# Performance work log

Measured on AMD Instinct MI355X. Metric: run time of the kernel, lower is better.

Reference implementation:

```python
import jax, jax.numpy as jnp
import numpy as np

B, T_CACHE, N_STATE, N_HEAD = 128, 448, 1280, 20
HEAD_DIM = N_STATE // N_HEAD


def setup_inputs() -> dict:
    key = jax.random.key(0)
    ks = jax.random.split(key, 10)
    s = 1.0 / np.sqrt(N_STATE)
    return {
        "x": jax.random.normal(ks[0], (B, 1, N_STATE), jnp.float32),
        "k_cache": jax.random.normal(ks[1], (B, T_CACHE, N_STATE), jnp.float32),
        "v_cache": jax.random.normal(ks[2], (B, T_CACHE, N_STATE), jnp.float32),
        "mask": jnp.zeros((1, T_CACHE), jnp.float32),
        "Wq": jax.random.normal(ks[3], (N_STATE, N_STATE), jnp.float32) * s,
        "bq": jax.random.normal(ks[4], (N_STATE,), jnp.float32) * s,
        "Wk": jax.random.normal(ks[5], (N_STATE, N_STATE), jnp.float32) * s,
        "Wv": jax.random.normal(ks[6], (N_STATE, N_STATE), jnp.float32) * s,
        "bv": jax.random.normal(ks[7], (N_STATE,), jnp.float32) * s,
        "Wo": jax.random.normal(ks[8], (N_STATE, N_STATE), jnp.float32) * s,
        "bo": jax.random.normal(ks[9], (N_STATE,), jnp.float32) * s,
    }


def reference(x, k_cache, v_cache, mask, Wq, bq, Wk, Wv, bv, Wo, bo):
    b, q_len, n_state = x.shape  # q_len == 1 in loop (streaming) mode
    h, d = N_HEAD, n_state // N_HEAD

    # Q/K/V projections (Whisper: key has no bias)
    q = x @ Wq + bq                         # [B, 1, n_state]
    k = x @ Wk                              # [B, 1, n_state]
    v = x @ Wv + bv                         # [B, 1, n_state]

    # streaming KV-cache shift-and-append
    k_cache = jnp.concatenate([k_cache[:, 1:, :], k], axis=1)  # [B, T, n_state]
    v_cache = jnp.concatenate([v_cache[:, 1:, :], v], axis=1)

    t = k_cache.shape[1]
    scale = d ** (-0.25)
    qh = q.reshape(b, q_len, h, d).transpose(0, 2, 1, 3) * scale   # [B, H, q, d]
    kh = k_cache.reshape(b, t, h, d).transpose(0, 2, 3, 1) * scale  # [B, H, d, T]
    vh = v_cache.reshape(b, t, h, d).transpose(0, 2, 1, 3)          # [B, H, T, d]

    qk = jnp.matmul(qh, kh) + mask          # [B, H, q, T]
    qk = qk.astype(jnp.float32)
    w = jax.nn.softmax(qk, axis=-1).astype(qh.dtype)
    wv = jnp.matmul(w, vh)                  # [B, H, q, d]
    wv = wv.transpose(0, 2, 1, 3).reshape(b, q_len, n_state)

    out = wv @ Wo + bo                      # [B, q, n_state]
    return out, k_cache, v_cache
```

## Files before the change

kernel.cpp:

```cpp
#include <hip/hip_runtime.h>
#include <cstddef>

#define NSTATE 1280
#define TCACHE 448
#define NBATCH 128
#define NHEAD  20
#define HDIM   64
#define NT     8
#define RPC    (TCACHE / NT)

typedef float f4 __attribute__((ext_vector_type(4)));

__device__ __forceinline__ void gemm_body(const float* __restrict__ A,
                                          const float* __restrict__ B,
                                          const float* __restrict__ bias,
                                          float* __restrict__ C, size_t ldc,
                                          int kb, int ke, float scale)
{
    __shared__ float As[32][64];
    __shared__ float Bs[32][32];
    const int tid = threadIdx.x;
    const int m0 = blockIdx.y * 64;
    const int n0 = blockIdx.x * 32;
    const int tr = tid >> 4;
    const int tc = tid & 15;
    float acc[4][2] = {{0.f,0.f},{0.f,0.f},{0.f,0.f},{0.f,0.f}};

    for (int k0 = kb; k0 < ke; k0 += 32) {
        #pragma unroll
        for (int j = 0; j < 2; ++j) {
            int chunk = tid * 2 + j;
            int row   = chunk >> 3;
            int kc    = (chunk & 7) << 2;
            float4 a = *(const float4*)(A + (size_t)(m0 + row) * NSTATE + k0 + kc);
            As[kc+0][row] = a.x; As[kc+1][row] = a.y;
            As[kc+2][row] = a.z; As[kc+3][row] = a.w;
        }
        {
            int row = tid >> 3;
            int nc  = (tid & 7) << 2;
            float4 b4 = *(const float4*)(B + (size_t)(k0 + row) * NSTATE + n0 + nc);
            *(float4*)&Bs[row][nc] = b4;
        }
        __syncthreads();
        #pragma unroll
        for (int kk = 0; kk < 32; ++kk) {
            float4 a = *(const float4*)&As[kk][tr << 2];
            float2 b = *(const float2*)&Bs[kk][tc << 1];
            acc[0][0] = fmaf(a.x, b.x, acc[0][0]); acc[0][1] = fmaf(a.x, b.y, acc[0][1]);
            acc[1][0] = fmaf(a.y, b.x, acc[1][0]); acc[1][1] = fmaf(a.y, b.y, acc[1][1]);
            acc[2][0] = fmaf(a.z, b.x, acc[2][0]); acc[2][1] = fmaf(a.z, b.y, acc[2][1]);
            acc[3][0] = fmaf(a.w, b.x, acc[3][0]); acc[3][1] = fmaf(a.w, b.y, acc[3][1]);
        }
        __syncthreads();
    }
    const int n = n0 + (tc << 1);
    const float b0 = bias ? bias[n]   : 0.f;
    const float b1 = bias ? bias[n+1] : 0.f;
    #pragma unroll
    for (int i = 0; i < 4; ++i) {
        size_t m = (size_t)(m0 + (tr << 2) + i);
        C[m * ldc + n]     = (acc[i][0] + b0) * scale;
        C[m * ldc + n + 1] = (acc[i][1] + b1) * scale;
    }
}

__global__ void __launch_bounds__(256) proj_qkv_kernel(
    const float* __restrict__ x,
    const float* __restrict__ Wq, const float* __restrict__ bq,
    const float* __restrict__ Wk,
    const float* __restrict__ Wv, const float* __restrict__ bv,
    float* __restrict__ q_ws, float* __restrict__ kout, float* __restrict__ vout)
{
    const int z = blockIdx.z;
    if (z == 0) {
        gemm_body(x, Wq, bq, q_ws, NSTATE, 0, NSTATE, 0.125f);
    } else if (z == 1) {
        gemm_body(x, Wk, nullptr, kout + (size_t)(TCACHE-1) * NSTATE,
                  (size_t)TCACHE * NSTATE, 0, NSTATE, 1.0f);
    } else {
        gemm_body(x, Wv, bv, vout + (size_t)(TCACHE-1) * NSTATE,
                  (size_t)TCACHE * NSTATE, 0, NSTATE, 1.0f);
    }
}

__global__ void __launch_bounds__(320) scorek_kernel(
    const float* __restrict__ kin, const float* __restrict__ q_ws,
    const float* __restrict__ mask, float* __restrict__ kout,
    float* __restrict__ sc_ws)
{
    const int tc = blockIdx.x, b = blockIdx.y;
    const int tid = threadIdx.x;
    const int h = tid >> 4;
    const int col = tid << 2;
    const size_t base = (size_t)b * TCACHE * NSTATE;
    const float4 q4 = *(const float4*)(q_ws + (size_t)b * NSTATE + col);
    const int t0 = tc * RPC;
    const int nrows = (tc == NT - 1) ? RPC - 1 : RPC;
    const float* src0 = kin + base + (size_t)(t0 + 1) * NSTATE + col;
    float* dst0 = kout + base + (size_t)t0 * NSTATE + col;
    float* scrow = sc_ws + ((size_t)b * NHEAD + h) * TCACHE + t0;

    #pragma unroll 4
    for (int r = 0; r < nrows; ++r) {
        f4 kv = __builtin_nontemporal_load((const f4*)(src0 + (size_t)r * NSTATE));
        __builtin_nontemporal_store(kv, (f4*)(dst0 + (size_t)r * NSTATE));
        float p = kv[0]*q4.x + kv[1]*q4.y + kv[2]*q4.z + kv[3]*q4.w;
        p += __shfl_xor(p, 1); p += __shfl_xor(p, 2);
        p += __shfl_xor(p, 4); p += __shfl_xor(p, 8);
        if ((tid & 15) == 0) scrow[r] = p + mask[t0 + r];
    }
    if (tc == NT - 1) {
        const f4 kv = *(const f4*)(kout + base + (size_t)(TCACHE-1) * NSTATE + col);
        float p = kv[0]*q4.x + kv[1]*q4.y + kv[2]*q4.z + kv[3]*q4.w;
        p += __shfl_xor(p, 1); p += __shfl_xor(p, 2);
        p += __shfl_xor(p, 4); p += __shfl_xor(p, 8);
        if ((tid & 15) == 0) scrow[RPC - 1] = p + mask[TCACHE - 1];
    }
}

__global__ void __launch_bounds__(320) pvv_kernel(
    const float* __restrict__ vin, const float* __restrict__ sc_ws,
    float* __restrict__ vout, float* __restrict__ wvp)
{
    const int tc = blockIdx.x, b = blockIdx.y;
    const int tid = threadIdx.x;
    const int h = tid >> 4, l = tid & 15;
    const int col = tid << 2;
    const int t0 = tc * RPC;
    __shared__ float wl[NHEAD * RPC];

    const float* row = sc_ws + ((size_t)b * NHEAD + h) * TCACHE;
    float v[28];
    float m = -1e30f;
    #pragma unroll
    for (int j = 0; j < 28; ++j) { v[j] = row[l + 16*j]; m = fmaxf(m, v[j]); }
    #pragma unroll
    for (int d = 1; d <= 8; d <<= 1) m = fmaxf(m, __shfl_xor(m, d));
    float s = 0.f;
    #pragma unroll
    for (int j = 0; j < 28; ++j) s += __expf(v[j] - m);
    #pragma unroll
    for (int d = 1; d <= 8; d <<= 1) s += __shfl_xor(s, d);
    const float inv = 1.0f / s;
    #pragma unroll
    for (int j = 0; j < 4; ++j) {
        int r = l + 16*j;
        if (r < RPC) wl[h * RPC + r] = __expf(row[t0 + r] - m) * inv;
    }
    __syncthreads();

    const size_t base = (size_t)b * TCACHE * NSTATE;
    const int nrows = (tc == NT - 1) ? RPC - 1 : RPC;
    const float* src0 = vin + base + (size_t)(t0 + 1) * NSTATE + col;
    float* dst0 = vout + base + (size_t)t0 * NSTATE + col;
    float ax = 0.f, ay = 0.f, az = 0.f, aw = 0.f;
    #pragma unroll 4
    for (int r = 0; r < nrows; ++r) {
        f4 vv = __builtin_nontemporal_load((const f4*)(src0 + (size_t)r * NSTATE));
        __builtin_nontemporal_store(vv, (f4*)(dst0 + (size_t)r * NSTATE));
        const float w = wl[h * RPC + r];
        ax = fmaf(w, vv[0], ax); ay = fmaf(w, vv[1], ay);
        az = fmaf(w, vv[2], az); aw = fmaf(w, vv[3], aw);
    }
    if (tc == NT - 1) {
        const f4 vv = *(const f4*)(vout + base + (size_t)(TCACHE-1) * NSTATE + col);
        const float w = wl[h * RPC + RPC - 1];
        ax = fmaf(w, vv[0], ax); ay = fmaf(w, vv[1], ay);
        az = fmaf(w, vv[2], az); aw = fmaf(w, vv[3], aw);
    }
    *(float4*)(wvp + ((size_t)b * NT + tc) * NSTATE + col) =
        make_float4(ax, ay, az, aw);
}

__global__ void __launch_bounds__(256) wv_reduce_kernel(
    const float* __restrict__ wvp, float* __restrict__ wv_ws)
{
    const size_t idx = ((size_t)blockIdx.x * 256 + threadIdx.x) * 4;
    const int b = (int)(idx / NSTATE), col = (int)(idx % NSTATE);
    float4 s = make_float4(0.f, 0.f, 0.f, 0.f);
    #pragma unroll
    for (int c = 0; c < NT; ++c) {
        float4 a = *(const float4*)(wvp + ((size_t)b * NT + c) * NSTATE + col);
        s.x += a.x; s.y += a.y; s.z += a.z; s.w += a.w;
    }
    *(float4*)(wv_ws + idx) = s;
}

__global__ void __launch_bounds__(256) outproj_kernel(
    const float* __restrict__ wv, const float* __restrict__ Wo,
    float* __restrict__ po)
{
    const int sp = blockIdx.z;
    gemm_body(wv, Wo, nullptr, po + (size_t)sp * NBATCH * NSTATE,
              NSTATE, sp * 320, sp * 320 + 320, 1.0f);
}

__global__ void __launch_bounds__(256) out_reduce_kernel(
    const float* __restrict__ po, const float* __restrict__ bo,
    float* __restrict__ out)
{
    const size_t idx = ((size_t)blockIdx.x * 256 + threadIdx.x) * 4;
    const int col = (int)(idx % NSTATE);
    float4 s = *(const float4*)(bo + col);
    #pragma unroll
    for (int c = 0; c < 4; ++c) {
        float4 a = *(const float4*)(po + (size_t)c * NBATCH * NSTATE + idx);
        s.x += a.x; s.y += a.y; s.z += a.z; s.w += a.w;
    }
    *(float4*)(out + idx) = s;
}

extern "C" void kernel_launch(void* const* d_in, const int* in_sizes, int n_in,
                              void* d_out, int out_size, void* d_ws, size_t ws_size,
                              hipStream_t stream)
{
    const float* x       = (const float*)d_in[0];
    const float* k_cache = (const float*)d_in[1];
    const float* v_cache = (const float*)d_in[2];
    const float* mask    = (const float*)d_in[3];
    const float* Wq      = (const float*)d_in[4];
    const float* bq      = (const float*)d_in[5];
    const float* Wk      = (const float*)d_in[6];
    const float* Wv      = (const float*)d_in[7];
    const float* bv      = (const float*)d_in[8];
    const float* Wo      = (const float*)d_in[9];
    const float* bo      = (const float*)d_in[10];

    float* out  = (float*)d_out;
    float* kout = out + (size_t)NBATCH * NSTATE;
    float* vout = kout + (size_t)NBATCH * TCACHE * NSTATE;

    float* ws     = (float*)d_ws;
    float* q_ws   = ws;
    float* sc_ws  = q_ws  + (size_t)NBATCH * NSTATE;
    float* wvp_ws = sc_ws + (size_t)NBATCH * NHEAD * TCACHE;
    float* po_ws  = wvp_ws + (size_t)NBATCH * NT * NSTATE;
    float* wv_ws  = po_ws + (size_t)4 * NBATCH * NSTATE;

    proj_qkv_kernel<<<dim3(40, 2, 3), 256, 0, stream>>>(x, Wq, bq, Wk, Wv, bv,
                                                        q_ws, kout, vout);
    scorek_kernel<<<dim3(NT, NBATCH), 320, 0, stream>>>(k_cache, q_ws, mask,
                                                        kout, sc_ws);
    pvv_kernel<<<dim3(NT, NBATCH), 320, 0, stream>>>(v_cache, sc_ws, vout, wvp_ws);
    wv_reduce_kernel<<<dim3(160), 256, 0, stream>>>(wvp_ws, wv_ws);
    outproj_kernel<<<dim3(40, 2, 4), 256, 0, stream>>>(wv_ws, Wo, po_ws);
    out_reduce_kernel<<<dim3(160), 256, 0, stream>>>(po_ws, bo, out);
}
```

Baseline: 317.6 us.

## Replace fp32 projection GEMMs with bf16 MFMA kernels using pre-transposed weights

```diff
diff --git a/kernel.cpp b/kernel.cpp
--- a/kernel.cpp
+++ b/kernel.cpp
@@ -10,78 +10,117 @@
 #define RPC    (TCACHE / NT)
 
 typedef float f4 __attribute__((ext_vector_type(4)));
-
-__device__ __forceinline__ void gemm_body(const float* __restrict__ A,
-                                          const float* __restrict__ B,
-                                          const float* __restrict__ bias,
-                                          float* __restrict__ C, size_t ldc,
-                                          int kb, int ke, float scale)
-{
-    __shared__ float As[32][64];
-    __shared__ float Bs[32][32];
-    const int tid = threadIdx.x;
-    const int m0 = blockIdx.y * 64;
-    const int n0 = blockIdx.x * 32;
-    const int tr = tid >> 4;
-    const int tc = tid & 15;
-    float acc[4][2] = {{0.f,0.f},{0.f,0.f},{0.f,0.f},{0.f,0.f}};
-
-    for (int k0 = kb; k0 < ke; k0 += 32) {
-        #pragma unroll
-        for (int j = 0; j < 2; ++j) {
-            int chunk = tid * 2 + j;
-            int row   = chunk >> 3;
-            int kc    = (chunk & 7) << 2;
-            float4 a = *(const float4*)(A + (size_t)(m0 + row) * NSTATE + k0 + kc);
-            As[kc+0][row] = a.x; As[kc+1][row] = a.y;
-            As[kc+2][row] = a.z; As[kc+3][row] = a.w;
-        }
-        {
-            int row = tid >> 3;
-            int nc  = (tid & 7) << 2;
-            float4 b4 = *(const float4*)(B + (size_t)(k0 + row) * NSTATE + n0 + nc);
-            *(float4*)&Bs[row][nc] = b4;
+typedef float f32x4 __attribute__((ext_vector_type(4)));
+typedef short bf16x8 __attribute__((ext_vector_type(8)));
+typedef unsigned short u16;
+
+__device__ __forceinline__ u16 f2bf(float f) {
+    unsigned u = __builtin_bit_cast(unsigned, f);
+    u += 0x7fff + ((u >> 16) & 1);
+    return (u16)(u >> 16);
+}
+
+__global__ void __launch_bounds__(256) cvt_kernel(
+    const float* __restrict__ Wq, const float* __restrict__ Wk,
+    const float* __restrict__ Wv, const float* __restrict__ Wo,
+    const float* __restrict__ x, u16* __restrict__ WT, u16* __restrict__ xbf)
+{
+    const int z = blockIdx.z;
+    const int t = threadIdx.x;
+    const int r = t >> 2;
+    const int c0 = (t & 3) << 4;
+    if (z < 4) {
+        const float* src = (z == 0) ? Wq : (z == 1) ? Wk : (z == 2) ? Wv : Wo;
+        u16* dst = WT + (size_t)z * NSTATE * NSTATE;
+        const int k0 = blockIdx.x * 64, n0 = blockIdx.y * 64;
+        __shared__ u16 tile[64][65];
+        #pragma unroll
+        for (int j = 0; j < 16; j += 4) {
+            float4 v = *(const float4*)(src + (size_t)(k0 + r) * NSTATE + n0 + c0 + j);
+            tile[c0 + j + 0][r] = f2bf(v.x);
+            tile[c0 + j + 1][r] = f2bf(v.y);
+            tile[c0 + j + 2][r] = f2bf(v.z);
+            tile[c0 + j + 3][r] = f2bf(v.w);
         }
         __syncthreads();
-        #pragma unroll
-        for (int kk = 0; kk < 32; ++kk) {
-            float4 a = *(const float4*)&As[kk][tr << 2];
-            float2 b = *(const float2*)&Bs[kk][tc << 1];
-            acc[0][0] = fmaf(a.x, b.x, acc[0][0]); acc[0][1] = fmaf(a.x, b.y, acc[0][1]);
-            acc[1][0] = fmaf(a.y, b.x, acc[1][0]); acc[1][1] = fmaf(a.y, b.y, acc[1][1]);
-            acc[2][0] = fmaf(a.z, b.x, acc[2][0]); acc[2][1] = fmaf(a.z, b.y, acc[2][1]);
-            acc[3][0] = fmaf(a.w, b.x, acc[3][0]); acc[3][1] = fmaf(a.w, b.y, acc[3][1]);
-        }
-        __syncthreads();
-    }
-    const int n = n0 + (tc << 1);
-    const float b0 = bias ? bias[n]   : 0.f;
-    const float b1 = bias ? bias[n+1] : 0.f;
-    #pragma unroll
-    for (int i = 0; i < 4; ++i) {
-        size_t m = (size_t)(m0 + (tr << 2) + i);
-        C[m * ldc + n]     = (acc[i][0] + b0) * scale;
-        C[m * ldc + n + 1] = (acc[i][1] + b1) * scale;
-    }
-}
-
-__global__ void __launch_bounds__(256) proj_qkv_kernel(
-    const float* __restrict__ x,
-    const float* __restrict__ Wq, const float* __restrict__ bq,
-    const float* __restrict__ Wk,
-    const float* __restrict__ Wv, const float* __restrict__ bv,
+        u16* o = dst + (size_t)(n0 + r) * NSTATE + k0 + c0;
+        #pragma unroll
+        for (int j = 0; j < 16; ++j) o[j] = tile[r][c0 + j];
+    } else {
+        if (blockIdx.y >= 2) return;
+        const int k0 = blockIdx.x * 64, m0 = blockIdx.y * 64;
+        u16* o = xbf + (size_t)(m0 + r) * NSTATE + k0 + c0;
+        #pragma unroll
+        for (int j = 0; j < 16; j += 4) {
+            float4 v = *(const float4*)(x + (size_t)(m0 + r) * NSTATE + k0 + c0 + j);
+            o[j + 0] = f2bf(v.x); o[j + 1] = f2bf(v.y);
+            o[j + 2] = f2bf(v.z); o[j + 3] = f2bf(v.w);
+        }
+    }
+}
+
+__device__ __forceinline__ void mfma_gemm(const u16* __restrict__ A,
+                                          const u16* __restrict__ Wrow,
+                                          f32x4 acc[8], int l)
+{
+    const int kg = l >> 4;
+    const int ra = l & 15;
+    #pragma unroll 2
+    for (int ks = 0; ks < NSTATE; ks += 32) {
+        const int kk = ks + kg * 8;
+        bf16x8 b = *(const bf16x8*)(Wrow + kk);
+        #pragma unroll
+        for (int mf = 0; mf < 8; ++mf) {
+            bf16x8 a = *(const bf16x8*)(A + (size_t)(mf * 16 + ra) * NSTATE + kk);
+            acc[mf] = __builtin_amdgcn_mfma_f32_16x16x32_bf16(a, b, acc[mf], 0, 0, 0);
+        }
+    }
+}
+
+__global__ void __launch_bounds__(256) proj_mfma_kernel(
+    const u16* __restrict__ xbf, const u16* __restrict__ WT,
+    const float* __restrict__ bq, const float* __restrict__ bv,
     float* __restrict__ q_ws, float* __restrict__ kout, float* __restrict__ vout)
 {
-    const int z = blockIdx.z;
-    if (z == 0) {
-        gemm_body(x, Wq, bq, q_ws, NSTATE, 0, NSTATE, 0.125f);
-    } else if (z == 1) {
-        gemm_body(x, Wk, nullptr, kout + (size_t)(TCACHE-1) * NSTATE,
-                  (size_t)TCACHE * NSTATE, 0, NSTATE, 1.0f);
-    } else {
-        gemm_body(x, Wv, bv, vout + (size_t)(TCACHE-1) * NSTATE,
-                  (size_t)TCACHE * NSTATE, 0, NSTATE, 1.0f);
-    }
+    const int nt = blockIdx.x, z = blockIdx.y;
+    const int w = threadIdx.x >> 6, l = threadIdx.x & 63;
+    const int col = nt * 64 + w * 16 + (l & 15);
+    const int kg = l >> 4;
+    const u16* Wrow = WT + (size_t)z * NSTATE * NSTATE + (size_t)col * NSTATE;
+    f32x4 acc[8] = {};
+    mfma_gemm(xbf, Wrow, acc, l);
+
+    const float bias = (z == 0) ? bq[col] : (z == 2) ? bv[col] : 0.f;
+    #pragma unroll
+    for (int mf = 0; mf < 8; ++mf) {
+        #pragma unroll
+        for (int j = 0; j < 4; ++j) {
+            const int m = mf * 16 + kg * 4 + j;
+            const float val = acc[mf][j] + bias;
+            if (z == 0)      q_ws[(size_t)m * NSTATE + col] = val * 0.125f;
+            else if (z == 1) kout[((size_t)m * TCACHE + TCACHE - 1) * NSTATE + col] = val;
+            else             vout[((size_t)m * TCACHE + TCACHE - 1) * NSTATE + col] = val;
+        }
+    }
+}
+
+__global__ void __launch_bounds__(256) outproj_mfma_kernel(
+    const u16* __restrict__ wvbf, const u16* __restrict__ WT,
+    const float* __restrict__ bo, float* __restrict__ out)
+{
+    const int nt = blockIdx.x;
+    const int w = threadIdx.x >> 6, l = threadIdx.x & 63;
+    const int col = nt * 64 + w * 16 + (l & 15);
+    const int kg = l >> 4;
+    const u16* Wrow = WT + (size_t)3 * NSTATE * NSTATE + (size_t)col * NSTATE;
+    f32x4 acc[8] = {};
+    mfma_gemm(wvbf, Wrow, acc, l);
+    const float bias = bo[col];
+    #pragma unroll
+    for (int mf = 0; mf < 8; ++mf)
+        #pragma unroll
+        for (int j = 0; j < 4; ++j)
+            out[(size_t)(mf * 16 + kg * 4 + j) * NSTATE + col] = acc[mf][j] + bias;
 }
 
 __global__ void __launch_bounds__(320) scorek_kernel(
@@ -174,7 +213,7 @@
 }
 
 __global__ void __launch_bounds__(256) wv_reduce_kernel(
-    const float* __restrict__ wvp, float* __restrict__ wv_ws)
+    const float* __restrict__ wvp, u16* __restrict__ wvbf)
 {
     const size_t idx = ((size_t)blockIdx.x * 256 + threadIdx.x) * 4;
     const int b = (int)(idx / NSTATE), col = (int)(idx % NSTATE);
@@ -184,31 +223,8 @@
         float4 a = *(const float4*)(wvp + ((size_t)b * NT + c) * NSTATE + col);
         s.x += a.x; s.y += a.y; s.z += a.z; s.w += a.w;
     }
-    *(float4*)(wv_ws + idx) = s;
-}
-
-__global__ void __launch_bounds__(256) outproj_kernel(
-    const float* __restrict__ wv, const float* __restrict__ Wo,
-    float* __restrict__ po)
-{
-    const int sp = blockIdx.z;
-    gemm_body(wv, Wo, nullptr, po + (size_t)sp * NBATCH * NSTATE,
-              NSTATE, sp * 320, sp * 320 + 320, 1.0f);
-}
-
-__global__ void __launch_bounds__(256) out_reduce_kernel(
-    const float* __restrict__ po, const float* __restrict__ bo,
-    float* __restrict__ out)
-{
-    const size_t idx = ((size_t)blockIdx.x * 256 + threadIdx.x) * 4;
-    const int col = (int)(idx % NSTATE);
-    float4 s = *(const float4*)(bo + col);
-    #pragma unroll
-    for (int c = 0; c < 4; ++c) {
-        float4 a = *(const float4*)(po + (size_t)c * NBATCH * NSTATE + idx);
-        s.x += a.x; s.y += a.y; s.z += a.z; s.w += a.w;
-    }
-    *(float4*)(out + idx) = s;
+    u16* o = wvbf + idx;
+    o[0] = f2bf(s.x); o[1] = f2bf(s.y); o[2] = f2bf(s.z); o[3] = f2bf(s.w);
 }
 
 extern "C" void kernel_launch(void* const* d_in, const int* in_sizes, int n_in,
@@ -235,15 +251,16 @@
     float* q_ws   = ws;
     float* sc_ws  = q_ws  + (size_t)NBATCH * NSTATE;
     float* wvp_ws = sc_ws + (size_t)NBATCH * NHEAD * TCACHE;
-    float* po_ws  = wvp_ws + (size_t)NBATCH * NT * NSTATE;
-    float* wv_ws  = po_ws + (size_t)4 * NBATCH * NSTATE;
-
-    proj_qkv_kernel<<<dim3(40, 2, 3), 256, 0, stream>>>(x, Wq, bq, Wk, Wv, bv,
-                                                        q_ws, kout, vout);
+    u16*   WT     = (u16*)(wvp_ws + (size_t)NBATCH * NT * NSTATE);
+    u16*   xbf    = WT + (size_t)4 * NSTATE * NSTATE;
+    u16*   wvbf   = xbf + (size_t)NBATCH * NSTATE;
+
+    cvt_kernel<<<dim3(20, 20, 5), 256, 0, stream>>>(Wq, Wk, Wv, Wo, x, WT, xbf);
+    proj_mfma_kernel<<<dim3(20, 3), 256, 0, stream>>>(xbf, WT, bq, bv,
+                                                      q_ws, kout, vout);
     scorek_kernel<<<dim3(NT, NBATCH), 320, 0, stream>>>(k_cache, q_ws, mask,
                                                         kout, sc_ws);
     pvv_kernel<<<dim3(NT, NBATCH), 320, 0, stream>>>(v_cache, sc_ws, vout, wvp_ws);
-    wv_reduce_kernel<<<dim3(160), 256, 0, stream>>>(wvp_ws, wv_ws);
-    outproj_kernel<<<dim3(40, 2, 4), 256, 0, stream>>>(wv_ws, Wo, po_ws);
-    out_reduce_kernel<<<dim3(160), 256, 0, stream>>>(po_ws, bo, out);
-}
+    wv_reduce_kernel<<<dim3(160), 256, 0, stream>>>(wvp_ws, wvbf);
+    outproj_mfma_kernel<<<dim3(20), 256, 0, stream>>>(wvbf, WT, bo, out);
+}
```

New measurement: 344.7 us. +8.5%, slower.

## Fuse score and PV streaming kernels with split-softmax combine

Applied to the files above, without the earlier changes.

```diff
diff --git a/kernel.cpp b/kernel.cpp
--- a/kernel.cpp
+++ b/kernel.cpp
@@ -84,107 +84,132 @@
     }
 }
 
-__global__ void __launch_bounds__(320) scorek_kernel(
-    const float* __restrict__ kin, const float* __restrict__ q_ws,
-    const float* __restrict__ mask, float* __restrict__ kout,
-    float* __restrict__ sc_ws)
-{
-    const int tc = blockIdx.x, b = blockIdx.y;
-    const int tid = threadIdx.x;
-    const int h = tid >> 4;
-    const int col = tid << 2;
-    const size_t base = (size_t)b * TCACHE * NSTATE;
-    const float4 q4 = *(const float4*)(q_ws + (size_t)b * NSTATE + col);
-    const int t0 = tc * RPC;
-    const int nrows = (tc == NT - 1) ? RPC - 1 : RPC;
-    const float* src0 = kin + base + (size_t)(t0 + 1) * NSTATE + col;
-    float* dst0 = kout + base + (size_t)t0 * NSTATE + col;
-    float* scrow = sc_ws + ((size_t)b * NHEAD + h) * TCACHE + t0;
-
-    #pragma unroll 4
-    for (int r = 0; r < nrows; ++r) {
-        f4 kv = __builtin_nontemporal_load((const f4*)(src0 + (size_t)r * NSTATE));
-        __builtin_nontemporal_store(kv, (f4*)(dst0 + (size_t)r * NSTATE));
-        float p = kv[0]*q4.x + kv[1]*q4.y + kv[2]*q4.z + kv[3]*q4.w;
-        p += __shfl_xor(p, 1); p += __shfl_xor(p, 2);
-        p += __shfl_xor(p, 4); p += __shfl_xor(p, 8);
-        if ((tid & 15) == 0) scrow[r] = p + mask[t0 + r];
-    }
-    if (tc == NT - 1) {
-        const f4 kv = *(const f4*)(kout + base + (size_t)(TCACHE-1) * NSTATE + col);
-        float p = kv[0]*q4.x + kv[1]*q4.y + kv[2]*q4.z + kv[3]*q4.w;
-        p += __shfl_xor(p, 1); p += __shfl_xor(p, 2);
-        p += __shfl_xor(p, 4); p += __shfl_xor(p, 8);
-        if ((tid & 15) == 0) scrow[RPC - 1] = p + mask[TCACHE - 1];
-    }
-}
-
-__global__ void __launch_bounds__(320) pvv_kernel(
-    const float* __restrict__ vin, const float* __restrict__ sc_ws,
-    float* __restrict__ vout, float* __restrict__ wvp)
+__global__ void __launch_bounds__(320) fused_stream_kernel(
+    const float* __restrict__ kin, const float* __restrict__ vin,
+    const float* __restrict__ q_ws, const float* __restrict__ mask,
+    float* __restrict__ kout, float* __restrict__ vout,
+    float* __restrict__ pvp, float* __restrict__ m_ws, float* __restrict__ s_ws)
 {
     const int tc = blockIdx.x, b = blockIdx.y;
     const int tid = threadIdx.x;
     const int h = tid >> 4, l = tid & 15;
     const int col = tid << 2;
+    const size_t base = (size_t)b * TCACHE * NSTATE;
     const int t0 = tc * RPC;
-    __shared__ float wl[NHEAD * RPC];
-
-    const float* row = sc_ws + ((size_t)b * NHEAD + h) * TCACHE;
-    float v[28];
-    float m = -1e30f;
-    #pragma unroll
-    for (int j = 0; j < 28; ++j) { v[j] = row[l + 16*j]; m = fmaxf(m, v[j]); }
-    #pragma unroll
-    for (int d = 1; d <= 8; d <<= 1) m = fmaxf(m, __shfl_xor(m, d));
-    float s = 0.f;
-    #pragma unroll
-    for (int j = 0; j < 28; ++j) s += __expf(v[j] - m);
-    #pragma unroll
-    for (int d = 1; d <= 8; d <<= 1) s += __shfl_xor(s, d);
-    const float inv = 1.0f / s;
-    #pragma unroll
-    for (int j = 0; j < 4; ++j) {
-        int r = l + 16*j;
-        if (r < RPC) wl[h * RPC + r] = __expf(row[t0 + r] - m) * inv;
+    const int nrows = (tc == NT - 1) ? RPC - 1 : RPC;
+
+    __shared__ float sc[NHEAD][RPC];
+
+    const float4 q4 = *(const float4*)(q_ws + (size_t)b * NSTATE + col);
+
+    {
+        const float* src0 = kin + base + (size_t)(t0 + 1) * NSTATE + col;
+        float* dst0 = kout + base + (size_t)t0 * NSTATE + col;
+        #pragma unroll 4
+        for (int r = 0; r < nrows; ++r) {
+            f4 kv = __builtin_nontemporal_load((const f4*)(src0 + (size_t)r * NSTATE));
+            __builtin_nontemporal_store(kv, (f4*)(dst0 + (size_t)r * NSTATE));
+            float p = kv[0]*q4.x + kv[1]*q4.y + kv[2]*q4.z + kv[3]*q4.w;
+            p += __shfl_xor(p, 1); p += __shfl_xor(p, 2);
+            p += __shfl_xor(p, 4); p += __shfl_xor(p, 8);
+            if (l == 0) sc[h][r] = p + mask[t0 + r];
+        }
+        if (tc == NT - 1) {
+            const f4 kv = *(const f4*)(kout + base + (size_t)(TCACHE-1) * NSTATE + col);
+            float p = kv[0]*q4.x + kv[1]*q4.y + kv[2]*q4.z + kv[3]*q4.w;
+            p += __shfl_xor(p, 1); p += __shfl_xor(p, 2);
+            p += __shfl_xor(p, 4); p += __shfl_xor(p, 8);
+            if (l == 0) sc[h][RPC - 1] = p + mask[TCACHE - 1];
+        }
     }
     __syncthreads();
 
-    const size_t base = (size_t)b * TCACHE * NSTATE;
-    const int nrows = (tc == NT - 1) ? RPC - 1 : RPC;
-    const float* src0 = vin + base + (size_t)(t0 + 1) * NSTATE + col;
-    float* dst0 = vout + base + (size_t)t0 * NSTATE + col;
+    {
+        float v[4];
+        float m = -1e30f;
+        #pragma unroll
+        for (int j = 0; j < 4; ++j) {
+            int r = l + 16 * j;
+            v[j] = (r < RPC) ? sc[h][r] : -1e30f;
+            m = fmaxf(m, v[j]);
+        }
+        #pragma unroll
+        for (int d = 1; d <= 8; d <<= 1) m = fmaxf(m, __shfl_xor(m, d));
+        float s = 0.f;
+        #pragma unroll
+        for (int j = 0; j < 4; ++j) {
+            v[j] = __expf(v[j] - m);
+            s += v[j];
+        }
+        #pragma unroll
+        for (int d = 1; d <= 8; d <<= 1) s += __shfl_xor(s, d);
+        __syncthreads();
+        #pragma unroll
+        for (int j = 0; j < 4; ++j) {
+            int r = l + 16 * j;
+            if (r < RPC) sc[h][r] = v[j];
+        }
+        if (l == 0) {
+            m_ws[((size_t)b * NT + tc) * NHEAD + h] = m;
+            s_ws[((size_t)b * NT + tc) * NHEAD + h] = s;
+        }
+    }
+    __syncthreads();
+
     float ax = 0.f, ay = 0.f, az = 0.f, aw = 0.f;
-    #pragma unroll 4
-    for (int r = 0; r < nrows; ++r) {
-        f4 vv = __builtin_nontemporal_load((const f4*)(src0 + (size_t)r * NSTATE));
-        __builtin_nontemporal_store(vv, (f4*)(dst0 + (size_t)r * NSTATE));
-        const float w = wl[h * RPC + r];
-        ax = fmaf(w, vv[0], ax); ay = fmaf(w, vv[1], ay);
-        az = fmaf(w, vv[2], az); aw = fmaf(w, vv[3], aw);
-    }
-    if (tc == NT - 1) {
-        const f4 vv = *(const f4*)(vout + base + (size_t)(TCACHE-1) * NSTATE + col);
-        const float w = wl[h * RPC + RPC - 1];
-        ax = fmaf(w, vv[0], ax); ay = fmaf(w, vv[1], ay);
-        az = fmaf(w, vv[2], az); aw = fmaf(w, vv[3], aw);
-    }
-    *(float4*)(wvp + ((size_t)b * NT + tc) * NSTATE + col) =
+    {
+        const float* src0 = vin + base + (size_t)(t0 + 1) * NSTATE + col;
+        float* dst0 = vout + base + (size_t)t0 * NSTATE + col;
+        #pragma unroll 4
+        for (int r = 0; r < nrows; ++r) {
+            f4 vv = __builtin_nontemporal_load((const f4*)(src0 + (size_t)r * NSTATE));
+            __builtin_nontemporal_store(vv, (f4*)(dst0 + (size_t)r * NSTATE));
+            const float w = sc[h][r];
+            ax = fmaf(w, vv[0], ax); ay = fmaf(w, vv[1], ay);
+            az = fmaf(w, vv[2], az); aw = fmaf(w, vv[3], aw);
+        }
+        if (tc == NT - 1) {
+            const f4 vv = *(const f4*)(vout + base + (size_t)(TCACHE-1) * NSTATE + col);
+            const float w = sc[h][RPC - 1];
+            ax = fmaf(w, vv[0], ax); ay = fmaf(w, vv[1], ay);
+            az = fmaf(w, vv[2], az); aw = fmaf(w, vv[3], aw);
+        }
+    }
+    *(float4*)(pvp + ((size_t)b * NT + tc) * NSTATE + col) =
         make_float4(ax, ay, az, aw);
 }
 
-__global__ void __launch_bounds__(256) wv_reduce_kernel(
-    const float* __restrict__ wvp, float* __restrict__ wv_ws)
+__global__ void __launch_bounds__(256) combine_kernel(
+    const float* __restrict__ pvp, const float* __restrict__ m_ws,
+    const float* __restrict__ s_ws, float* __restrict__ wv_ws)
 {
     const size_t idx = ((size_t)blockIdx.x * 256 + threadIdx.x) * 4;
     const int b = (int)(idx / NSTATE), col = (int)(idx % NSTATE);
-    float4 s = make_float4(0.f, 0.f, 0.f, 0.f);
+    const int h = col >> 6;
+
+    float m[NT], s[NT];
+    float M = -1e30f;
     #pragma unroll
     for (int c = 0; c < NT; ++c) {
-        float4 a = *(const float4*)(wvp + ((size_t)b * NT + c) * NSTATE + col);
-        s.x += a.x; s.y += a.y; s.z += a.z; s.w += a.w;
-    }
-    *(float4*)(wv_ws + idx) = s;
+        m[c] = m_ws[((size_t)b * NT + c) * NHEAD + h];
+        s[c] = s_ws[((size_t)b * NT + c) * NHEAD + h];
+        M = fmaxf(M, m[c]);
+    }
+    float S = 0.f;
+    float f[NT];
+    #pragma unroll
+    for (int c = 0; c < NT; ++c) { f[c] = __expf(m[c] - M); S += s[c] * f[c]; }
+    const float inv = 1.0f / S;
+
+    float4 acc = make_float4(0.f, 0.f, 0.f, 0.f);
+    #pragma unroll
+    for (int c = 0; c < NT; ++c) {
+        const float w = f[c] * inv;
+        float4 a = *(const float4*)(pvp + ((size_t)b * NT + c) * NSTATE + col);
+        acc.x = fmaf(w, a.x, acc.x); acc.y = fmaf(w, a.y, acc.y);
+        acc.z = fmaf(w, a.z, acc.z); acc.w = fmaf(w, a.w, acc.w);
+    }
+    *(float4*)(wv_ws + idx) = acc;
 }
 
 __global__ void __launch_bounds__(256) outproj_kernel(
@@ -233,17 +258,17 @@
 
     float* ws     = (float*)d_ws;
     float* q_ws   = ws;
-    float* sc_ws  = q_ws  + (size_t)NBATCH * NSTATE;
-    float* wvp_ws = sc_ws + (size_t)NBATCH * NHEAD * TCACHE;
-    float* po_ws  = wvp_ws + (size_t)NBATCH * NT * NSTATE;
-    float* wv_ws  = po_ws + (size_t)4 * NBATCH * NSTATE;
+    float* pvp_ws = q_ws  + (size_t)NBATCH * NSTATE;
+    float* m_ws   = pvp_ws + (size_t)NBATCH * NT * NSTATE;
+    float* s_ws   = m_ws  + (size_t)NBATCH * NT * NHEAD;
+    float* wv_ws  = s_ws  + (size_t)NBATCH * NT * NHEAD;
+    float* po_ws  = wv_ws + (size_t)NBATCH * NSTATE;
 
     proj_qkv_kernel<<<dim3(40, 2, 3), 256, 0, stream>>>(x, Wq, bq, Wk, Wv, bv,
                                                         q_ws, kout, vout);
-    scorek_kernel<<<dim3(NT, NBATCH), 320, 0, stream>>>(k_cache, q_ws, mask,
-                                                        kout, sc_ws);
-    pvv_kernel<<<dim3(NT, NBATCH), 320, 0, stream>>>(v_cache, sc_ws, vout, wvp_ws);
-    wv_reduce_kernel<<<dim3(160), 256, 0, stream>>>(wvp_ws, wv_ws);
+    fused_stream_kernel<<<dim3(NT, NBATCH), 320, 0, stream>>>(
+        k_cache, v_cache, q_ws, mask, kout, vout, pvp_ws, m_ws, s_ws);
+    combine_kernel<<<dim3(160), 256, 0, stream>>>(pvp_ws, m_ws, s_ws, wv_ws);
     outproj_kernel<<<dim3(40, 2, 4), 256, 0, stream>>>(wv_ws, Wo, po_ws);
     out_reduce_kernel<<<dim3(160), 256, 0, stream>>>(po_ws, bo, out);
 }
```

Result: faster. 308.4 us (-2.9%).
